# Performance work log

Measured on AMD Instinct MI355X. Metric: run time of the kernel, lower is better.

## Reference

```python
import jax, jax.numpy as jnp
import numpy as np

NUM_HEADS = 8
LN_EPS = 1e-5


def layer_norm(x, g, b):
    mu = jnp.mean(x, axis=-1, keepdims=True)
    var = jnp.mean(jnp.square(x - mu), axis=-1, keepdims=True)
    return (x - mu) / jnp.sqrt(var + LN_EPS) * g + b


def setup_inputs() -> dict:
    key = jax.random.key(0)
    ks = jax.random.split(key, 16)
    B, N, D, F = 16, 1024, 256, 1024
    s = 0.02
    return {
        "x": jax.random.normal(ks[0], (B, N, D), jnp.float32),
        "spatial_encoding": jax.random.normal(ks[1], (B, N, N), jnp.float32),
        "edge_encoding": jax.random.normal(ks[2], (B, N, N), jnp.float32),
        "gamma1": jnp.ones((D,), jnp.float32),
        "beta1": jnp.zeros((D,), jnp.float32),
        "gamma2": jnp.ones((D,), jnp.float32),
        "beta2": jnp.zeros((D,), jnp.float32),
        "Wq": jax.random.normal(ks[3], (D, D), jnp.float32) * s,
        "Wk": jax.random.normal(ks[4], (D, D), jnp.float32) * s,
        "Wv": jax.random.normal(ks[5], (D, D), jnp.float32) * s,
        "Wo": jax.random.normal(ks[6], (D, D), jnp.float32) * s,
        "W1": jax.random.normal(ks[7], (F, D), jnp.float32) * s,
        "b1": jnp.zeros((F,), jnp.float32),
        "W2": jax.random.normal(ks[8], (D, F), jnp.float32) * s,
        "b2": jnp.zeros((D,), jnp.float32),
    }


def reference(x, spatial_encoding, edge_encoding, gamma1, beta1, gamma2, beta2,
              Wq, Wk, Wv, Wo, W1, b1, W2, b2):
    B, N, D = x.shape
    H = NUM_HEADS
    hd = D // H
    scale = D ** (-0.5)  # source scales by hidden_dim, not head_size

    att_in = layer_norm(x, gamma1, beta1)

    def proj(W):  # [B,N,D] -> [B,H,N,hd]
        return (att_in @ W.T).reshape(B, N, H, hd).transpose(0, 2, 1, 3)

    q, k, v = proj(Wq), proj(Wk), proj(Wv)
    bias = (spatial_encoding + edge_encoding)[:, None]  # [B,1,N,N]
    a = jnp.einsum('bhnd,bhmd->bhnm', q, k) * scale + bias
    pad_mask = jnp.any(a != 0, axis=-1)  # [B,H,N]
    a = jnp.where(pad_mask[..., None], a, -jnp.inf)
    p = jnp.nan_to_num(jax.nn.softmax(a, axis=-1))
    o = jnp.einsum('bhnm,bhmd->bhnd', p, v)
    attn = o.transpose(0, 2, 1, 3).reshape(B, N, D) @ Wo.T
    att_output = attn + x

    pad_mask2 = jnp.any(att_output == 0, axis=-1)  # [B,N]
    ffn_in = layer_norm(x, gamma2, beta2)  # note: norm of x per the source
    h = jax.nn.gelu(ffn_in @ W1.T + b1, approximate=True)
    ffn_out = h @ W2.T + b2 + att_output
    return jnp.where(pad_mask2[..., None], 0.0, ffn_out)
```

## Files before the change

### kernel.cpp

```cpp
#include <hip/hip_runtime.h>
#include <hip/hip_bf16.h>
#include <math.h>

#define Bq 16
#define Nq 1024
#define Dq 256
#define Fq 1024
#define Hq 8
#define HDq 32
#define Mq (Bq * Nq)
#define SCALE 0.0625f
#define LN_EPS 1e-5f

typedef __attribute__((ext_vector_type(8))) short short8;
typedef __attribute__((ext_vector_type(4))) float f32x4;

__device__ __forceinline__ float bf2f(unsigned short s) {
    unsigned u = ((unsigned)s) << 16;
    return __builtin_bit_cast(float, u);
}
__device__ __forceinline__ unsigned short f2bf(float f) {
    __hip_bfloat16 h = __float2bfloat16(f);
    return __builtin_bit_cast(unsigned short, h);
}

typedef __attribute__((address_space(3))) unsigned int lds_uint;
typedef const __attribute__((address_space(1))) unsigned int glb_uint;
__device__ __forceinline__ void async16(void* lds, const void* g) {
    __builtin_amdgcn_global_load_lds((glb_uint*)g, (lds_uint*)lds, 16, 0, 0);
}

__device__ __forceinline__ float gelu_tanh(float v) {
    const float c = 0.7978845608028654f;
    float u = c * (v + 0.044715f * v * v * v);
    return 0.5f * v * (1.0f + tanhf(u));
}

__global__ __launch_bounds__(256) void cvt_weights(
    const float* __restrict__ Wq, const float* __restrict__ Wk,
    const float* __restrict__ Wv, const float* __restrict__ Wo,
    const float* __restrict__ W1, const float* __restrict__ W2,
    unsigned short* __restrict__ dst)
{
    const int blk = blockIdx.x;
    int seg, local;
    if (blk < 256)      { seg = blk >> 6; local = blk & 63; }
    else if (blk < 512) { seg = 4; local = blk - 256; }
    else                { seg = 5; local = blk - 512; }
    const float* srcs[6] = {Wq, Wk, Wv, Wo, W1, W2};
    const size_t dsto[6] = {0, 65536, 131072, 196608, 262144, 524288};
    const float* src = srcs[seg] + (size_t)local * 1024;
    unsigned short* d = dst + dsto[seg] + (size_t)local * 1024;
    const int t4 = threadIdx.x * 4;
    float4 v = *(const float4*)(src + t4);
    uint2 o;
    o.x = (unsigned)f2bf(v.x) | ((unsigned)f2bf(v.y) << 16);
    o.y = (unsigned)f2bf(v.z) | ((unsigned)f2bf(v.w) << 16);
    *(uint2*)(d + t4) = o;
}

__global__ __launch_bounds__(256) void ln2_kernel(
    const float* __restrict__ x,
    const float* __restrict__ g1, const float* __restrict__ bb1,
    const float* __restrict__ g2, const float* __restrict__ bb2,
    unsigned short* __restrict__ att_in, unsigned short* __restrict__ ffn_in)
{
    const int row = blockIdx.x;
    const int t = threadIdx.x;
    const size_t base = (size_t)row * Dq;
    float v = x[base + t];

    float s = v, sq = v * v;
    #pragma unroll
    for (int off = 32; off > 0; off >>= 1) {
        s  += __shfl_down(s, off);
        sq += __shfl_down(sq, off);
    }
    __shared__ float ssum[4], ssq[4];
    __shared__ float mu_s, rstd_s;
    const int lane = t & 63, wid = t >> 6;
    if (lane == 0) { ssum[wid] = s; ssq[wid] = sq; }
    __syncthreads();
    if (t == 0) {
        float S = ssum[0] + ssum[1] + ssum[2] + ssum[3];
        float Q = ssq[0] + ssq[1] + ssq[2] + ssq[3];
        float mu = S * (1.0f / Dq);
        float var = Q * (1.0f / Dq) - mu * mu;
        mu_s = mu;
        rstd_s = rsqrtf(var + LN_EPS);
    }
    __syncthreads();
    const float nx = (v - mu_s) * rstd_s;
    att_in[base + t] = f2bf(nx * g1[t] + bb1[t]);
    ffn_in[base + t] = f2bf(nx * g2[t] + bb2[t]);
}

#define TM 128
#define TN 128
#define TK 32

__global__ __launch_bounds__(256) void gemm_mfma(
    const unsigned short* __restrict__ A, const unsigned short* __restrict__ W,
    const float* __restrict__ bias, const float* __restrict__ add,
    float* __restrict__ outF, unsigned short* __restrict__ outBF,
    unsigned short* __restrict__ Qb, unsigned short* __restrict__ Kb,
    unsigned short* __restrict__ Vt,
    int M, int Nc, int K, int mode, int apply_gelu)
{
    __shared__ unsigned short As[TM * TK];
    __shared__ unsigned short Bs[TN * TK];
    const int t = threadIdx.x;
    const int w = t >> 6, lane = t & 63;
    const int col = lane & 15, quad = lane >> 4;
    const int wr = w >> 1, wc = w & 1;
    const int row0 = blockIdx.y * TM;
    const int col0 = blockIdx.x * TN;

    f32x4 acc[4][4] = {};

    for (int k0 = 0; k0 < K; k0 += TK) {
        #pragma unroll
        for (int j = 0; j < 2; j++) {
            const int c = w * 128 + j * 64 + lane;
            const int r = c >> 2, seg = c & 3;
            async16(&As[(size_t)(w * 128 + j * 64) * 8],
                    A + (size_t)(row0 + r) * K + k0 + seg * 8);
            async16(&Bs[(size_t)(w * 128 + j * 64) * 8],
                    W + (size_t)(col0 + r) * K + k0 + seg * 8);
        }
        __syncthreads();
        short8 wf[4], af[4];
        #pragma unroll
        for (int i = 0; i < 4; i++)
            wf[i] = *(const short8*)&Bs[(wc * 64 + i * 16 + col) * TK + quad * 8];
        #pragma unroll
        for (int j = 0; j < 4; j++)
            af[j] = *(const short8*)&As[(wr * 64 + j * 16 + col) * TK + quad * 8];
        #pragma unroll
        for (int i = 0; i < 4; i++)
            #pragma unroll
            for (int j = 0; j < 4; j++)
                acc[i][j] = __builtin_amdgcn_mfma_f32_16x16x32_bf16(wf[i], af[j], acc[i][j], 0, 0, 0);
        __syncthreads();
    }

    #pragma unroll
    for (int i = 0; i < 4; i++) {
        #pragma unroll
        for (int j = 0; j < 4; j++) {
            const int c0 = col0 + wc * 64 + i * 16 + quad * 4;
            const int r  = row0 + wr * 64 + j * 16 + col;
            float4 v = make_float4(acc[i][j][0], acc[i][j][1], acc[i][j][2], acc[i][j][3]);
            if (mode == 2 && c0 < 256) { v.x *= SCALE; v.y *= SCALE; v.z *= SCALE; v.w *= SCALE; }
            if (bias) {
                float4 bb = *(const float4*)&bias[c0];
                v.x += bb.x; v.y += bb.y; v.z += bb.z; v.w += bb.w;
            }
            if (apply_gelu) {
                v.x = gelu_tanh(v.x); v.y = gelu_tanh(v.y);
                v.z = gelu_tanh(v.z); v.w = gelu_tanh(v.w);
            }
            if (add) {
                float4 aa = *(const float4*)&add[(size_t)r * Nc + c0];
                v.x += aa.x; v.y += aa.y; v.z += aa.z; v.w += aa.w;
            }
            if (mode == 0) {
                *(float4*)&outF[(size_t)r * Nc + c0] = v;
            } else if (mode == 1) {
                uint2 o;
                o.x = (unsigned)f2bf(v.x) | ((unsigned)f2bf(v.y) << 16);
                o.y = (unsigned)f2bf(v.z) | ((unsigned)f2bf(v.w) << 16);
                *(uint2*)&outBF[(size_t)r * Nc + c0] = o;
            } else {
                const int b = r >> 10, n = r & 1023;
                if (c0 < 512) {
                    const int cq = c0 & 255;
                    const int h = cq >> 5, d0 = cq & 31;
                    unsigned short* dst = (c0 < 256 ? Qb : Kb);
                    uint2 o;
                    o.x = (unsigned)f2bf(v.x) | ((unsigned)f2bf(v.y) << 16);
                    o.y = (unsigned)f2bf(v.z) | ((unsigned)f2bf(v.w) << 16);
                    *(uint2*)&dst[(((size_t)(b * Hq + h) << 10) + n) * HDq + d0] = o;
                } else {
                    const int cv = c0 - 512;
                    const int h = cv >> 5, d0 = cv & 31;
                    unsigned short* dst = Vt + (((size_t)(b * Hq + h) * HDq + d0) << 10) + n;
                    dst[0]      = f2bf(v.x);
                    dst[1024]   = f2bf(v.y);
                    dst[2048]   = f2bf(v.z);
                    dst[3072]   = f2bf(v.w);
                }
            }
        }
    }
}

#define SSTR2 1032

__global__ __launch_bounds__(256) void attn_mfma(
    const unsigned short* __restrict__ Qbf, const unsigned short* __restrict__ Kbf,
    const unsigned short* __restrict__ Vt, const float* __restrict__ sp,
    const float* __restrict__ ed, unsigned short* __restrict__ O16)
{
    const int b = blockIdx.y;
    const int n0 = blockIdx.x * 16;
    const int t = threadIdx.x;
    const int w = t >> 6;
    const int lane = t & 63;
    const int col = lane & 15;
    const int quad = lane >> 4;

    __shared__ unsigned short bias16[16][SSTR2];
    __shared__ unsigned short S16T[16][SSTR2];
    __shared__ float Ored[4][16][34];
    __shared__ float wsum[4][16];
    __shared__ float inv_row[16];

    {
        const float* spb = sp + ((size_t)b * Nq + n0) * Nq;
        const float* edb = ed + ((size_t)b * Nq + n0) * Nq;
        for (int i = t; i < 4096; i += 256) {
            const int r = i >> 8;
            const int c4 = i & 255;
            float4 a = *(const float4*)(spb + (size_t)r * Nq + c4 * 4);
            float4 e = *(const float4*)(edb + (size_t)r * Nq + c4 * 4);
            uint2 o;
            o.x = (unsigned)f2bf(a.x + e.x) | ((unsigned)f2bf(a.y + e.y) << 16);
            o.y = (unsigned)f2bf(a.z + e.z) | ((unsigned)f2bf(a.w + e.w) << 16);
            *(uint2*)&bias16[r][c4 * 4] = o;
        }
    }
    __syncthreads();

    const size_t bbase = (size_t)b * Hq;
    for (int h = 0; h < Hq; h++) {
        const unsigned short* Qh = Qbf + (bbase + h) * Nq * HDq;
        const unsigned short* Kh = Kbf + (bbase + h) * Nq * HDq;
        const unsigned short* Vth = Vt + (bbase + h) * HDq * Nq;

        short8 aq = *(const short8*)(Qh + (size_t)(n0 + col) * HDq + quad * 8);

        float rsum[4] = {0.f, 0.f, 0.f, 0.f};

        for (int mt = w; mt < 64; mt += 4) {
            const int m0 = mt * 16;
            short8 bk = *(const short8*)(Kh + (size_t)(m0 + col) * HDq + quad * 8);
            f32x4 cc = {0.f, 0.f, 0.f, 0.f};
            cc = __builtin_amdgcn_mfma_f32_16x16x32_bf16(aq, bk, cc, 0, 0, 0);
            #pragma unroll
            for (int i = 0; i < 4; i++) {
                const int r = quad * 4 + i;
                float s = cc[i] + bf2f(bias16[r][m0 + col]);
                float e = __expf(s);
                rsum[i] += e;
                S16T[r][m0 + col] = f2bf(e);
            }
        }
        #pragma unroll
        for (int off = 1; off < 16; off <<= 1) {
            #pragma unroll
            for (int i = 0; i < 4; i++)
                rsum[i] += __shfl_xor(rsum[i], off, 16);
        }
        if (col == 0) {
            #pragma unroll
            for (int i = 0; i < 4; i++) wsum[w][quad * 4 + i] = rsum[i];
        }
        __syncthreads();
        if (t < 16)
            inv_row[t] = 1.0f / (wsum[0][t] + wsum[1][t] + wsum[2][t] + wsum[3][t]);
        __syncthreads();

        f32x4 o0 = {0.f, 0.f, 0.f, 0.f}, o1 = {0.f, 0.f, 0.f, 0.f};
        for (int mt = 0; mt < 8; mt++) {
            const int m0 = w * 256 + mt * 32;
            short8 ap = *(const short8*)&S16T[col][m0 + quad * 8];
            short8 bv0 = *(const short8*)(Vth + (size_t)col * Nq + m0 + quad * 8);
            short8 bv1 = *(const short8*)(Vth + (size_t)(col + 16) * Nq + m0 + quad * 8);
            o0 = __builtin_amdgcn_mfma_f32_16x16x32_bf16(ap, bv0, o0, 0, 0, 0);
            o1 = __builtin_amdgcn_mfma_f32_16x16x32_bf16(ap, bv1, o1, 0, 0, 0);
        }
        #pragma unroll
        for (int i = 0; i < 4; i++) {
            const float inv = inv_row[quad * 4 + i];
            Ored[w][quad * 4 + i][col]      = o0[i] * inv;
            Ored[w][quad * 4 + i][col + 16] = o1[i] * inv;
        }
        __syncthreads();
        {
            const int q = t >> 4, d = t & 15;
            float v0 = Ored[0][q][d] + Ored[1][q][d] + Ored[2][q][d] + Ored[3][q][d];
            float v1 = Ored[0][q][d + 16] + Ored[1][q][d + 16] + Ored[2][q][d + 16] + Ored[3][q][d + 16];
            unsigned short* op = O16 + ((size_t)b * Nq + n0 + q) * Dq + h * HDq;
            op[d] = f2bf(v0);
            op[d + 16] = f2bf(v1);
        }
    }
}

__global__ __launch_bounds__(256) void pad2_kernel(
    const float* __restrict__ AO, float* __restrict__ out)
{
    const int row = blockIdx.x;
    const int t = threadIdx.x;
    const float v = AO[(size_t)row * Dq + t];
    unsigned long long m = __ballot(v == 0.0f);
    __shared__ unsigned long long w[4];
    if ((t & 63) == 0) w[t >> 6] = m;
    __syncthreads();
    if ((w[0] | w[1] | w[2] | w[3]) != 0ULL)
        out[(size_t)row * Dq + t] = 0.0f;
}

extern "C" void kernel_launch(void* const* d_in, const int* in_sizes, int n_in,
                              void* d_out, int out_size, void* d_ws, size_t ws_size,
                              hipStream_t stream)
{
    const float* x      = (const float*)d_in[0];
    const float* sp     = (const float*)d_in[1];
    const float* ed     = (const float*)d_in[2];
    const float* gamma1 = (const float*)d_in[3];
    const float* beta1  = (const float*)d_in[4];
    const float* gamma2 = (const float*)d_in[5];
    const float* beta2  = (const float*)d_in[6];
    const float* Wq     = (const float*)d_in[7];
    const float* Wk     = (const float*)d_in[8];
    const float* Wv     = (const float*)d_in[9];
    const float* Wo     = (const float*)d_in[10];
    const float* W1     = (const float*)d_in[11];
    const float* b1     = (const float*)d_in[12];
    const float* W2     = (const float*)d_in[13];
    const float* b2     = (const float*)d_in[14];
    float* out = (float*)d_out;

    unsigned short* s = (unsigned short*)d_ws;
    const size_t MD = (size_t)Mq * Dq;
    unsigned short* att_in16 = s;
    unsigned short* ffn_in16 = s + MD;
    unsigned short* Qbf      = s + 2 * MD;
    unsigned short* Kbf      = s + 3 * MD;
    unsigned short* Vtb      = s + 4 * MD;
    unsigned short* W16      = s + 5 * MD;
    unsigned short* h16      = s + 5 * MD + 786432;
    unsigned short* O16      = att_in16;
    float*          AO       = (float*)Qbf;

    unsigned short* Wo16 = W16 + 196608;
    unsigned short* W116 = W16 + 262144;
    unsigned short* W216 = W16 + 524288;

    cvt_weights<<<768, 256, 0, stream>>>(Wq, Wk, Wv, Wo, W1, W2, W16);

    ln2_kernel<<<Mq, 256, 0, stream>>>(x, gamma1, beta1, gamma2, beta2, att_in16, ffn_in16);

    dim3 gQKV(768 / TN, Mq / TM);
    gemm_mfma<<<gQKV, 256, 0, stream>>>(att_in16, W16, nullptr, nullptr, nullptr, nullptr,
                                        Qbf, Kbf, Vtb, Mq, 768, Dq, 2, 0);

    attn_mfma<<<dim3(Nq / 16, Bq), 256, 0, stream>>>(Qbf, Kbf, Vtb, sp, ed, O16);

    dim3 gP(Dq / TN, Mq / TM);
    gemm_mfma<<<gP, 256, 0, stream>>>(O16, Wo16, nullptr, x, AO, nullptr,
                                      nullptr, nullptr, nullptr, Mq, Dq, Dq, 0, 0);

    dim3 gF1(Fq / TN, Mq / TM);
    gemm_mfma<<<gF1, 256, 0, stream>>>(ffn_in16, W116, b1, nullptr, nullptr, h16,
                                       nullptr, nullptr, nullptr, Mq, Fq, Dq, 1, 1);

    gemm_mfma<<<gP, 256, 0, stream>>>(h16, W216, b2, AO, out, nullptr,
                                      nullptr, nullptr, nullptr, Mq, Dq, Fq, 0, 0);

    pad2_kernel<<<Mq, 256, 0, stream>>>(AO, out);
}
```

Before: 460.4 us.

## Assign one wave per head in attention and stream softmax-PV per chunk

```diff
diff --git a/kernel.cpp b/kernel.cpp
--- a/kernel.cpp
+++ b/kernel.cpp
@@ -195,9 +195,9 @@
     }
 }
 
-#define SSTR2 1032
-
-__global__ __launch_bounds__(256) void attn_mfma(
+#define BSTR 1028
+
+__global__ __launch_bounds__(512, 4) void attn_mfma(
     const unsigned short* __restrict__ Qbf, const unsigned short* __restrict__ Kbf,
     const unsigned short* __restrict__ Vt, const float* __restrict__ sp,
     const float* __restrict__ ed, unsigned short* __restrict__ O16)
@@ -205,21 +205,18 @@
     const int b = blockIdx.y;
     const int n0 = blockIdx.x * 16;
     const int t = threadIdx.x;
-    const int w = t >> 6;
+    const int h = t >> 6;
     const int lane = t & 63;
     const int col = lane & 15;
     const int quad = lane >> 4;
 
-    __shared__ unsigned short bias16[16][SSTR2];
-    __shared__ unsigned short S16T[16][SSTR2];
-    __shared__ float Ored[4][16][34];
-    __shared__ float wsum[4][16];
-    __shared__ float inv_row[16];
+    __shared__ unsigned short bias16[16 * BSTR];
+    __shared__ unsigned short S16[8][16 * 128];
 
     {
         const float* spb = sp + ((size_t)b * Nq + n0) * Nq;
         const float* edb = ed + ((size_t)b * Nq + n0) * Nq;
-        for (int i = t; i < 4096; i += 256) {
+        for (int i = t; i < 4096; i += 512) {
             const int r = i >> 8;
             const int c4 = i & 255;
             float4 a = *(const float4*)(spb + (size_t)r * Nq + c4 * 4);
@@ -227,74 +224,64 @@
             uint2 o;
             o.x = (unsigned)f2bf(a.x + e.x) | ((unsigned)f2bf(a.y + e.y) << 16);
             o.y = (unsigned)f2bf(a.z + e.z) | ((unsigned)f2bf(a.w + e.w) << 16);
-            *(uint2*)&bias16[r][c4 * 4] = o;
+            *(uint2*)&bias16[r * BSTR + c4 * 4] = o;
         }
     }
     __syncthreads();
 
-    const size_t bbase = (size_t)b * Hq;
-    for (int h = 0; h < Hq; h++) {
-        const unsigned short* Qh = Qbf + (bbase + h) * Nq * HDq;
-        const unsigned short* Kh = Kbf + (bbase + h) * Nq * HDq;
-        const unsigned short* Vth = Vt + (bbase + h) * HDq * Nq;
-
-        short8 aq = *(const short8*)(Qh + (size_t)(n0 + col) * HDq + quad * 8);
-
-        float rsum[4] = {0.f, 0.f, 0.f, 0.f};
-
-        for (int mt = w; mt < 64; mt += 4) {
-            const int m0 = mt * 16;
+    const size_t hb = (size_t)b * Hq + h;
+    const unsigned short* Qh = Qbf + hb * (Nq * HDq);
+    const unsigned short* Kh = Kbf + hb * (Nq * HDq);
+    const unsigned short* Vh = Vt  + hb * (HDq * Nq);
+    unsigned short* Sw = &S16[h][0];
+
+    const short8 aq = *(const short8*)(Qh + (size_t)(n0 + col) * HDq + quad * 8);
+
+    f32x4 o0 = {0.f, 0.f, 0.f, 0.f}, o1 = {0.f, 0.f, 0.f, 0.f};
+    float rsum[4] = {0.f, 0.f, 0.f, 0.f};
+
+    for (int tt = 0; tt < 8; tt++) {
+        const int k0 = tt * 128;
+        #pragma unroll
+        for (int m = 0; m < 8; m++) {
+            const int m0 = k0 + m * 16;
             short8 bk = *(const short8*)(Kh + (size_t)(m0 + col) * HDq + quad * 8);
             f32x4 cc = {0.f, 0.f, 0.f, 0.f};
             cc = __builtin_amdgcn_mfma_f32_16x16x32_bf16(aq, bk, cc, 0, 0, 0);
             #pragma unroll
             for (int i = 0; i < 4; i++) {
                 const int r = quad * 4 + i;
-                float s = cc[i] + bf2f(bias16[r][m0 + col]);
+                float s = cc[i] + bf2f(bias16[r * BSTR + m0 + col]);
                 float e = __expf(s);
                 rsum[i] += e;
-                S16T[r][m0 + col] = f2bf(e);
-            }
-        }
-        #pragma unroll
-        for (int off = 1; off < 16; off <<= 1) {
-            #pragma unroll
-            for (int i = 0; i < 4; i++)
-                rsum[i] += __shfl_xor(rsum[i], off, 16);
-        }
-        if (col == 0) {
-            #pragma unroll
-            for (int i = 0; i < 4; i++) wsum[w][quad * 4 + i] = rsum[i];
-        }
-        __syncthreads();
-        if (t < 16)
-            inv_row[t] = 1.0f / (wsum[0][t] + wsum[1][t] + wsum[2][t] + wsum[3][t]);
-        __syncthreads();
-
-        f32x4 o0 = {0.f, 0.f, 0.f, 0.f}, o1 = {0.f, 0.f, 0.f, 0.f};
-        for (int mt = 0; mt < 8; mt++) {
-            const int m0 = w * 256 + mt * 32;
-            short8 ap = *(const short8*)&S16T[col][m0 + quad * 8];
-            short8 bv0 = *(const short8*)(Vth + (size_t)col * Nq + m0 + quad * 8);
-            short8 bv1 = *(const short8*)(Vth + (size_t)(col + 16) * Nq + m0 + quad * 8);
+                const int sidx = (r * 128 + m * 16 + col) ^ ((r & 7) << 3);
+                Sw[sidx] = f2bf(e);
+            }
+        }
+        #pragma unroll
+        for (int c = 0; c < 4; c++) {
+            const int ridx = (col * 128 + c * 32 + quad * 8) ^ ((col & 7) << 3);
+            short8 ap  = *(const short8*)&Sw[ridx];
+            short8 bv0 = *(const short8*)(Vh + (size_t)col * Nq + k0 + c * 32 + quad * 8);
+            short8 bv1 = *(const short8*)(Vh + (size_t)(col + 16) * Nq + k0 + c * 32 + quad * 8);
             o0 = __builtin_amdgcn_mfma_f32_16x16x32_bf16(ap, bv0, o0, 0, 0, 0);
             o1 = __builtin_amdgcn_mfma_f32_16x16x32_bf16(ap, bv1, o1, 0, 0, 0);
         }
-        #pragma unroll
-        for (int i = 0; i < 4; i++) {
-            const float inv = inv_row[quad * 4 + i];
-            Ored[w][quad * 4 + i][col]      = o0[i] * inv;
-            Ored[w][quad * 4 + i][col + 16] = o1[i] * inv;
-        }
-        __syncthreads();
-        {
-            const int q = t >> 4, d = t & 15;
-            float v0 = Ored[0][q][d] + Ored[1][q][d] + Ored[2][q][d] + Ored[3][q][d];
-            float v1 = Ored[0][q][d + 16] + Ored[1][q][d + 16] + Ored[2][q][d + 16] + Ored[3][q][d + 16];
-            unsigned short* op = O16 + ((size_t)b * Nq + n0 + q) * Dq + h * HDq;
-            op[d] = f2bf(v0);
-            op[d + 16] = f2bf(v1);
-        }
+    }
+
+    #pragma unroll
+    for (int off = 1; off < 16; off <<= 1) {
+        #pragma unroll
+        for (int i = 0; i < 4; i++) rsum[i] += __shfl_xor(rsum[i], off, 16);
+    }
+
+    unsigned short* op = O16 + ((size_t)b * Nq + n0) * Dq + h * HDq;
+    #pragma unroll
+    for (int i = 0; i < 4; i++) {
+        const float inv = 1.0f / rsum[i];
+        const int q = quad * 4 + i;
+        op[(size_t)q * Dq + col]      = f2bf(o0[i] * inv);
+        op[(size_t)q * Dq + col + 16] = f2bf(o1[i] * inv);
     }
 }
 
@@ -357,7 +344,7 @@
     gemm_mfma<<<gQKV, 256, 0, stream>>>(att_in16, W16, nullptr, nullptr, nullptr, nullptr,
                                         Qbf, Kbf, Vtb, Mq, 768, Dq, 2, 0);
 
-    attn_mfma<<<dim3(Nq / 16, Bq), 256, 0, stream>>>(Qbf, Kbf, Vtb, sp, ed, O16);
+    attn_mfma<<<dim3(Nq / 16, Bq), 512, 0, stream>>>(Qbf, Kbf, Vtb, sp, ed, O16);
 
     dim3 gP(Dq / TN, Mq / TM);
     gemm_mfma<<<gP, 256, 0, stream>>>(O16, Wo16, nullptr, x, AO, nullptr,
```

Measured after the change: 412.1 us. 1.12x faster.
